# Kernel tuning notes

Hardware: AMD Instinct MI355X
Metric: run time of the kernel (lower is better)

Reference implementation:

```python
import jax, jax.numpy as jnp
import numpy as np

B, D, F = 16384, 512, 28
GIN = D + D + F + 1  # 1053
EPS = 1e-5


def setup_inputs() -> dict:
    key = jax.random.key(0)
    ks = jax.random.split(key, 16)
    s = 0.02
    return {
        "team_embedding": jax.random.normal(ks[0], (B, D), jnp.float32),
        "opponent_embedding": jax.random.normal(ks[1], (B, D), jnp.float32),
        "game_features": jax.random.normal(ks[2], (B, F), jnp.float32),
        "won": jnp.round(jax.random.uniform(ks[3], (B, 1), jnp.float32)),
        # input_projection Linear(GIN -> D)
        "W_proj": jax.random.normal(ks[4], (D, GIN), jnp.float32) * s,
        "b_proj": jnp.zeros((D,), jnp.float32),
        # GRUCell params (PyTorch layout: [3D, *] with r,z,n blocks)
        "W_ih": jax.random.normal(ks[5], (3 * D, D), jnp.float32) * s,
        "b_ih": jnp.zeros((3 * D,), jnp.float32),
        "W_hh": jax.random.normal(ks[6], (3 * D, D), jnp.float32) * s,
        "b_hh": jnp.zeros((3 * D,), jnp.float32),
        # LayerNorm
        "gamma": jnp.ones((D,), jnp.float32),
        "beta": jnp.zeros((D,), jnp.float32),
        # game_importance MLP: D -> 128 -> 1
        "W_imp1": jax.random.normal(ks[7], (128, D), jnp.float32) * s,
        "b_imp1": jnp.zeros((128,), jnp.float32),
        "W_imp2": jax.random.normal(ks[8], (1, 128), jnp.float32) * s,
        "b_imp2": jnp.zeros((1,), jnp.float32),
    }


def reference(team_embedding, opponent_embedding, game_features, won,
              W_proj, b_proj, W_ih, b_ih, W_hh, b_hh,
              gamma, beta, W_imp1, b_imp1, W_imp2, b_imp2):
    # combined: [B, 2D+F+1]
    x = jnp.concatenate([team_embedding, opponent_embedding, game_features, won], axis=-1)
    # input_projection: Linear -> ReLU (Dropout is identity in eval)
    projected = jax.nn.relu(x @ W_proj.T + b_proj)  # [B, D]
    # game_importance: Linear -> ReLU -> Linear -> Sigmoid
    importance = jax.nn.sigmoid(jax.nn.relu(projected @ W_imp1.T + b_imp1) @ W_imp2.T + b_imp2)  # [B, 1]
    # GRUCell (PyTorch math)
    gi = projected @ W_ih.T + b_ih          # [B, 3D]
    gh = team_embedding @ W_hh.T + b_hh     # [B, 3D]
    i_r, i_z, i_n = jnp.split(gi, 3, axis=-1)
    h_r, h_z, h_n = jnp.split(gh, 3, axis=-1)
    r = jax.nn.sigmoid(i_r + h_r)
    z = jax.nn.sigmoid(i_z + h_z)
    n = jnp.tanh(i_n + r * h_n)
    new_embedding = (1.0 - z) * n + z * team_embedding
    # gated blend
    updated = team_embedding + importance * (new_embedding - team_embedding)
    # LayerNorm
    mu = jnp.mean(updated, axis=-1, keepdims=True)
    var = jnp.mean(jnp.square(updated - mu), axis=-1, keepdims=True)
    updated = gamma * (updated - mu) * jax.lax.rsqrt(var + EPS) + beta
    game_context = jax.lax.stop_gradient(projected)  # .detach().clone()
    return (updated, game_context)
```

## Files before the change

kernel.cpp:

```cpp
#include <hip/hip_runtime.h>
#include <hip/hip_bf16.h>


#define NB 16384
#define GINP 1088

typedef __bf16 bf16x8 __attribute__((ext_vector_type(8)));
typedef float f32x4 __attribute__((ext_vector_type(4)));
typedef unsigned short ushort8 __attribute__((ext_vector_type(8)));

__device__ __forceinline__ void gload_lds16(const void* g, void* l) {
  __builtin_amdgcn_global_load_lds(
      (const __attribute__((address_space(1))) void*)g,
      (__attribute__((address_space(3))) void*)l, 16, 0, 0);
}
__device__ __forceinline__ float sigmoidf_(float x) { return 1.0f / (1.0f + expf(-x)); }
__device__ __forceinline__ float bf2f(unsigned short u) {
  unsigned int x = ((unsigned int)u) << 16;
  float f; __builtin_memcpy(&f, &x, 4); return f;
}

__global__ __launch_bounds__(256) void prep_x2(
    const float* __restrict__ team, const float* __restrict__ opp,
    const float* __restrict__ gf, const float* __restrict__ won,
    __hip_bfloat16* __restrict__ X) {
  long idx = (long)blockIdx.x * 256 + threadIdx.x;
  if (idx >= (long)NB * 136) return;
  const int r = (int)(idx / 136);
  const int c8 = (int)(idx % 136) * 8;
  float v[8];
  if (c8 < 512) {
    float4 a = *(const float4*)&team[(size_t)r * 512 + c8];
    float4 b = *(const float4*)&team[(size_t)r * 512 + c8 + 4];
    v[0]=a.x; v[1]=a.y; v[2]=a.z; v[3]=a.w; v[4]=b.x; v[5]=b.y; v[6]=b.z; v[7]=b.w;
  } else if (c8 < 1024) {
    float4 a = *(const float4*)&opp[(size_t)r * 512 + (c8 - 512)];
    float4 b = *(const float4*)&opp[(size_t)r * 512 + (c8 - 512) + 4];
    v[0]=a.x; v[1]=a.y; v[2]=a.z; v[3]=a.w; v[4]=b.x; v[5]=b.y; v[6]=b.z; v[7]=b.w;
  } else if (c8 < 1048) {
    const int g0 = c8 - 1024;
#pragma unroll
    for (int e = 0; e < 8; ++e) v[e] = gf[(size_t)r * 28 + g0 + e];
  } else if (c8 == 1048) {
    v[0] = gf[(size_t)r * 28 + 24]; v[1] = gf[(size_t)r * 28 + 25];
    v[2] = gf[(size_t)r * 28 + 26]; v[3] = gf[(size_t)r * 28 + 27];
    v[4] = won[r]; v[5] = 0.f; v[6] = 0.f; v[7] = 0.f;
  } else {
#pragma unroll
    for (int e = 0; e < 8; ++e) v[e] = 0.f;
  }
  __hip_bfloat16 h[8];
#pragma unroll
  for (int e = 0; e < 8; ++e) h[e] = __float2bfloat16(v[e]);
  *(uint4*)&X[(size_t)r * GINP + c8] = *(const uint4*)h;
}

__global__ __launch_bounds__(256) void prep_w2(
    const float* __restrict__ Wproj, const float* __restrict__ Wih,
    const float* __restrict__ Whh, const float* __restrict__ Wimp1,
    const float* __restrict__ bih, const float* __restrict__ bhh,
    __hip_bfloat16* __restrict__ Wpb, __hip_bfloat16* __restrict__ Wrz,
    __hip_bfloat16* __restrict__ Wn, __hip_bfloat16* __restrict__ Wimp1b,
    float* __restrict__ bcat) {
  long idx = (long)blockIdx.x * 256 + threadIdx.x;
  if (idx < 512L * 1088) {
    int r = (int)(idx / 1088), c = (int)(idx % 1088);
    Wpb[idx] = __float2bfloat16(c < 1053 ? Wproj[(size_t)r * 1053 + c] : 0.f);
    return;
  }
  idx -= 512L * 1088;
  if (idx < 1024L * 1024) {
    int q = (int)(idx >> 10), c = (int)(idx & 1023);
    float v = (c < 512) ? Wih[(size_t)q * 512 + c] : Whh[(size_t)q * 512 + (c - 512)];
    Wrz[idx] = __float2bfloat16(v);
    return;
  }
  idx -= 1024L * 1024;
  if (idx < 1024L * 512) {
    int q = (int)(idx / 512), c = (int)(idx % 512);
    float v = (q < 512) ? Wih[(size_t)(1024 + q) * 512 + c]
                        : Whh[(size_t)(1024 + q - 512) * 512 + c];
    Wn[idx] = __float2bfloat16(v);
    return;
  }
  idx -= 1024L * 512;
  if (idx < 128L * 512) { Wimp1b[idx] = __float2bfloat16(Wimp1[idx]); return; }
  idx -= 128L * 512;
  if (idx < 2048) {
    int j = (int)idx;
    float v;
    if (j < 1024) v = bih[j] + bhh[j];
    else if (j < 1536) v = bih[j];
    else v = bhh[j - 512];
    bcat[j] = v;
  }
}

template <int MODE>
__global__ __launch_bounds__(512, 1) void gemm_dp(
    const __hip_bfloat16* __restrict__ A0, int lda0,
    const __hip_bfloat16* __restrict__ A1, int lda1,
    const __hip_bfloat16* __restrict__ W0, const __hip_bfloat16* __restrict__ W1,
    const float* __restrict__ bias,
    float* __restrict__ Cf, __hip_bfloat16* __restrict__ Cb,
    int tilesN, int NT0) {
  __shared__ __align__(16) unsigned short ldsA[3 * 256 * 64];
  __shared__ __align__(16) unsigned short ldsB[3 * 128 * 64];

  const int tid = threadIdx.x;
  const int wid = tid >> 6, lane = tid & 63;
  const int wr = wid >> 1, wc = wid & 1;
  const int fl = lane & 15, kh = lane >> 4;

  int bid = blockIdx.x;
  {
    const int cpx = gridDim.x >> 3;
    bid = (bid & 7) * cpx + (bid >> 3);
  }
  const int tm = bid / tilesN, tn = bid % tilesN;
  const int m0 = tm * 256;

  const __hip_bfloat16* Wp;
  int ldw, NT;
  if (MODE == 0) {
    Wp = W0 + (size_t)tn * 128 * GINP; ldw = GINP; NT = NT0;
  } else {
    if (tn < 8) { Wp = W0 + (size_t)tn * 128 * 1024; ldw = 1024; NT = 16; }
    else        { Wp = W1 + (size_t)(tn - 8) * 128 * 512; ldw = 512; NT = 8; }
  }
  const float* bp = bias + tn * 128;

  const int prow_b = tid >> 3;
  const int gp = tid & 7;

  auto stageAB = [&](int s, int buf) {
    const int kW = s * 64;
    const __hip_bfloat16* Ap; int lda; int kA;
    if (MODE == 0) { Ap = A0; lda = lda0; kA = s * 64; }
    else if (tn < 8) {
      if (s < 8) { Ap = A0; lda = lda0; kA = s * 64; }
      else       { Ap = A1; lda = lda1; kA = (s - 8) * 64; }
    } else if (tn < 12) { Ap = A0; lda = lda0; kA = s * 64; }
    else                { Ap = A1; lda = lda1; kA = s * 64; }
    unsigned short* la = &ldsA[buf * (256 * 64)];
    unsigned short* lb = &ldsB[buf * (128 * 64)];
#pragma unroll
    for (int i = 0; i < 4; ++i) {
      const int prow = i * 64 + prow_b;
      const int gl = gp ^ (prow & 7);
      gload_lds16(Ap + (size_t)(m0 + prow) * lda + kA + gl * 8,
                  la + i * 4096 + wid * 512);
    }
#pragma unroll
    for (int i = 0; i < 2; ++i) {
      const int prow = i * 64 + prow_b;
      const int gl = gp ^ (prow & 7);
      gload_lds16(Wp + (size_t)prow * ldw + kW + gl * 8,
                  lb + i * 4096 + wid * 512);
    }
  };

  f32x4 acc[4][4];
#pragma unroll
  for (int m = 0; m < 4; ++m)
#pragma unroll
    for (int n = 0; n < 4; ++n) acc[m][n] = (f32x4){0.f, 0.f, 0.f, 0.f};

  stageAB(0, 0);
  stageAB(1, 1);

  for (int t = 0; t < NT; ++t) {
    const int cur = t % 3;
    if (t + 1 < NT) {
      asm volatile("s_waitcnt vmcnt(6)" ::: "memory");
    } else {
      asm volatile("s_waitcnt vmcnt(0)" ::: "memory");
    }
    __builtin_amdgcn_s_barrier();
    if (t + 2 < NT) stageAB(t + 2, (t + 2) % 3);

    const unsigned short* At = &ldsA[cur * (256 * 64)];
    const unsigned short* Bt = &ldsB[cur * (128 * 64)];
    bf16x8 af[2][4], bfr[2][4];
#pragma unroll
    for (int kk = 0; kk < 2; ++kk) {
#pragma unroll
      for (int m = 0; m < 4; ++m) {
        const int r = wr * 64 + m * 16 + fl;
        const int g = (kk * 4 + kh) ^ (r & 7);
        af[kk][m] = *(const bf16x8*)&At[r * 64 + g * 8];
      }
#pragma unroll
      for (int n = 0; n < 4; ++n) {
        const int r = wc * 64 + n * 16 + fl;
        const int g = (kk * 4 + kh) ^ (r & 7);
        bfr[kk][n] = *(const bf16x8*)&Bt[r * 64 + g * 8];
      }
    }
    __builtin_amdgcn_s_setprio(1);
#pragma unroll
    for (int kk = 0; kk < 2; ++kk)
#pragma unroll
      for (int m = 0; m < 4; ++m)
#pragma unroll
        for (int n = 0; n < 4; ++n)
          acc[m][n] = __builtin_amdgcn_mfma_f32_16x16x32_bf16(af[kk][m], bfr[kk][n], acc[m][n], 0, 0, 0);
    __builtin_amdgcn_s_setprio(0);
  }

#pragma unroll
  for (int m = 0; m < 4; ++m)
#pragma unroll
    for (int n = 0; n < 4; ++n)
#pragma unroll
      for (int j = 0; j < 4; ++j) {
        const int lrow = wr * 64 + m * 16 + kh * 4 + j;
        const int lcol = wc * 64 + n * 16 + fl;
        const size_t grow = (size_t)(m0 + lrow);
        float v = acc[m][n][j] + bp[lcol];
        if (MODE == 0) {
          v = fmaxf(v, 0.f);
          Cf[grow * 512 + tn * 128 + lcol] = v;
          Cb[grow * 512 + tn * 128 + lcol] = __float2bfloat16(v);
        } else {
          Cb[grow * 2048 + tn * 128 + lcol] = __float2bfloat16(v);
        }
      }
}

__global__ __launch_bounds__(256, 2) void gemm_imp(
    const __hip_bfloat16* __restrict__ A, const __hip_bfloat16* __restrict__ W,
    const float* __restrict__ bias, float* __restrict__ Cf) {
  __shared__ __align__(16) unsigned short ldsA[128 * 64];
  __shared__ __align__(16) unsigned short ldsB[128 * 64];
  const int tid = threadIdx.x;
  const int w = tid >> 6, lane = tid & 63;
  const int wr = w >> 1, wc = w & 1;
  const int fl = lane & 15, kh = lane >> 4;
  const int srow = lane >> 3, scol = (lane & 7) * 8;
  const int m0 = blockIdx.x * 128;

  f32x4 acc[4][4];
#pragma unroll
  for (int m = 0; m < 4; ++m)
#pragma unroll
    for (int n = 0; n < 4; ++n) acc[m][n] = (f32x4){0.f, 0.f, 0.f, 0.f};

  for (int kt = 0; kt < 8; ++kt) {
    const int k0 = kt * 64;
#pragma unroll
    for (int c = 0; c < 4; ++c) {
      const int rgrp = c * 4 + w;
      const int row = rgrp * 8 + srow;
      gload_lds16(A + (size_t)(m0 + row) * 512 + k0 + scol, (char*)ldsA + rgrp * 1024);
      gload_lds16(W + (size_t)row * 512 + k0 + scol, (char*)ldsB + rgrp * 1024);
    }
    __syncthreads();
#pragma unroll
    for (int kk = 0; kk < 2; ++kk) {
      bf16x8 af[4], bfr[4];
#pragma unroll
      for (int m = 0; m < 4; ++m)
        af[m] = *(const bf16x8*)&ldsA[(wr * 64 + m * 16 + fl) * 64 + kk * 32 + kh * 8];
#pragma unroll
      for (int n = 0; n < 4; ++n)
        bfr[n] = *(const bf16x8*)&ldsB[(wc * 64 + n * 16 + fl) * 64 + kk * 32 + kh * 8];
#pragma unroll
      for (int m = 0; m < 4; ++m)
#pragma unroll
        for (int n = 0; n < 4; ++n)
          acc[m][n] = __builtin_amdgcn_mfma_f32_16x16x32_bf16(af[m], bfr[n], acc[m][n], 0, 0, 0);
    }
    __syncthreads();
  }
#pragma unroll
  for (int m = 0; m < 4; ++m)
#pragma unroll
    for (int n = 0; n < 4; ++n)
#pragma unroll
      for (int j = 0; j < 4; ++j) {
        const int lrow = wr * 64 + m * 16 + kh * 4 + j;
        const int lcol = wc * 64 + n * 16 + fl;
        if (lcol < 128)
          Cf[(size_t)(m0 + lrow) * 128 + lcol] = fmaxf(acc[m][n][j] + bias[lcol], 0.f);
      }
}

__global__ __launch_bounds__(256) void imp_k(const float* __restrict__ h1,
                                             const float* __restrict__ w2,
                                             const float* __restrict__ b2,
                                             float* __restrict__ imp) {
  const int row = blockIdx.x * 4 + (threadIdx.x >> 6);
  const int lane = threadIdx.x & 63;
  float p = h1[(size_t)row * 128 + lane] * w2[lane] +
            h1[(size_t)row * 128 + 64 + lane] * w2[64 + lane];
#pragma unroll
  for (int off = 32; off; off >>= 1) p += __shfl_down(p, off);
  if (lane == 0) imp[row] = sigmoidf_(p + b2[0]);
}

__global__ __launch_bounds__(256) void fuse_final2(
    const float* __restrict__ team, const __hip_bfloat16* __restrict__ gg,
    const float* __restrict__ imp, const float* __restrict__ gamma,
    const float* __restrict__ beta, float* __restrict__ out) {
  const int row = blockIdx.x * 4 + (threadIdx.x >> 6);
  const int lane = threadIdx.x & 63;
  const size_t gb = (size_t)row * 2048 + lane * 8;
  ushort8 sr = *(const ushort8*)&gg[gb];
  ushort8 szv = *(const ushort8*)&gg[gb + 512];
  ushort8 inn = *(const ushort8*)&gg[gb + 1024];
  ushort8 hnn = *(const ushort8*)&gg[gb + 1536];
  float4 t0 = *(const float4*)&team[(size_t)row * 512 + lane * 8];
  float4 t1 = *(const float4*)&team[(size_t)row * 512 + lane * 8 + 4];
  const float im = imp[row];
  float tv[8] = {t0.x, t0.y, t0.z, t0.w, t1.x, t1.y, t1.z, t1.w};
  float u[8];
  float s = 0.f, ss = 0.f;
#pragma unroll
  for (int e = 0; e < 8; ++e) {
    const float rg = sigmoidf_(bf2f(sr[e]));
    const float zg = sigmoidf_(bf2f(szv[e]));
    const float ng = tanhf(bf2f(inn[e]) + rg * bf2f(hnn[e]));
    const float ne = (1.f - zg) * ng + zg * tv[e];
    const float uu = tv[e] + im * (ne - tv[e]);
    u[e] = uu; s += uu; ss += uu * uu;
  }
#pragma unroll
  for (int off = 32; off; off >>= 1) {
    s += __shfl_down(s, off);
    ss += __shfl_down(ss, off);
  }
  s = __shfl(s, 0); ss = __shfl(ss, 0);
  const float mu = s * (1.f / 512.f);
  const float inv = rsqrtf(ss * (1.f / 512.f) - mu * mu + 1e-5f);
  float4 g0 = *(const float4*)&gamma[lane * 8], g1 = *(const float4*)&gamma[lane * 8 + 4];
  float4 b0 = *(const float4*)&beta[lane * 8], b1 = *(const float4*)&beta[lane * 8 + 4];
  float gv[8] = {g0.x, g0.y, g0.z, g0.w, g1.x, g1.y, g1.z, g1.w};
  float bv[8] = {b0.x, b0.y, b0.z, b0.w, b1.x, b1.y, b1.z, b1.w};
  float4 o0, o1;
  o0.x = gv[0] * (u[0] - mu) * inv + bv[0];
  o0.y = gv[1] * (u[1] - mu) * inv + bv[1];
  o0.z = gv[2] * (u[2] - mu) * inv + bv[2];
  o0.w = gv[3] * (u[3] - mu) * inv + bv[3];
  o1.x = gv[4] * (u[4] - mu) * inv + bv[4];
  o1.y = gv[5] * (u[5] - mu) * inv + bv[5];
  o1.z = gv[6] * (u[6] - mu) * inv + bv[6];
  o1.w = gv[7] * (u[7] - mu) * inv + bv[7];
  *(float4*)&out[(size_t)row * 512 + lane * 8] = o0;
  *(float4*)&out[(size_t)row * 512 + lane * 8 + 4] = o1;
}

extern "C" void kernel_launch(void* const* d_in, const int* in_sizes, int n_in,
                              void* d_out, int out_size, void* d_ws, size_t ws_size,
                              hipStream_t stream) {
  const float* team   = (const float*)d_in[0];
  const float* opp    = (const float*)d_in[1];
  const float* gf     = (const float*)d_in[2];
  const float* won    = (const float*)d_in[3];
  const float* W_proj = (const float*)d_in[4];
  const float* b_proj = (const float*)d_in[5];
  const float* W_ih   = (const float*)d_in[6];
  const float* b_ih   = (const float*)d_in[7];
  const float* W_hh   = (const float*)d_in[8];
  const float* b_hh   = (const float*)d_in[9];
  const float* gamma  = (const float*)d_in[10];
  const float* beta   = (const float*)d_in[11];
  const float* W_imp1 = (const float*)d_in[12];
  const float* b_imp1 = (const float*)d_in[13];
  const float* W_imp2 = (const float*)d_in[14];
  const float* b_imp2 = (const float*)d_in[15];

  char* ws = (char*)d_ws;
  size_t o = 0;
  __hip_bfloat16* Xbf    = (__hip_bfloat16*)(ws + o); o += (size_t)NB * GINP * 2;
  __hip_bfloat16* Wpb    = (__hip_bfloat16*)(ws + o); o += (size_t)512 * GINP * 2;
  __hip_bfloat16* Wrz    = (__hip_bfloat16*)(ws + o); o += (size_t)1024 * 1024 * 2;
  __hip_bfloat16* Wn     = (__hip_bfloat16*)(ws + o); o += (size_t)1024 * 512 * 2;
  __hip_bfloat16* Wimp1b = (__hip_bfloat16*)(ws + o); o += (size_t)128 * 512 * 2;
  float*          bcat   = (float*)(ws + o);          o += (size_t)2048 * 4;
  __hip_bfloat16* Pbf    = (__hip_bfloat16*)(ws + o); o += (size_t)NB * 512 * 2;
  float*          h1     = (float*)(ws + o);          o += (size_t)NB * 128 * 4;
  float*          imp    = (float*)(ws + o);          o += (size_t)NB * 4;
  __hip_bfloat16* gg     = (__hip_bfloat16*)(ws + o); o += (size_t)NB * 2048 * 2;

  float* out_updated = (float*)d_out;
  float* out_ctx     = (float*)d_out + (size_t)NB * 512;

  prep_x2<<<(NB * 136 + 255) / 256, 256, 0, stream>>>(team, opp, gf, won, Xbf);
  {
    const long total = 512L * 1088 + 1024L * 1024 + 1024L * 512 + 128L * 512 + 2048;
    prep_w2<<<(int)((total + 255) / 256), 256, 0, stream>>>(
        W_proj, W_ih, W_hh, W_imp1, b_ih, b_hh, Wpb, Wrz, Wn, Wimp1b, bcat);
  }
  gemm_dp<0><<<256, 512, 0, stream>>>(Xbf, GINP, nullptr, 0, Wpb, nullptr, b_proj,
                                      out_ctx, Pbf, 4, 17);
  gemm_imp<<<NB / 128, 256, 0, stream>>>(Pbf, Wimp1b, b_imp1, h1);
  imp_k<<<NB / 4, 256, 0, stream>>>(h1, W_imp2, b_imp2, imp);
  gemm_dp<2><<<1024, 512, 0, stream>>>(Pbf, 512, Xbf, GINP, Wrz, Wn, bcat,
                                       nullptr, gg, 16, 0);
  fuse_final2<<<NB / 4, 256, 0, stream>>>(team, gg, imp, gamma, beta, out_updated);
}
```

Before: 177.0 us.

## Enlarge GEMM tiles to 256x256 with 8-phase interleaved load/MFMA schedule

Both GEMM launches now use 256x256 output tiles instead of 256x128, with 8 waves in a 2x4 layout and 128 accumulator floats per thread. The main loop is double-buffered and split into four sub-phases, each interleaving LDS fragment reads, partial global-to-LDS staging of the next tiles, and a quarter of the MFMAs, with barriers between phases. The aim is more data reuse per LDS byte and better overlap of memory traffic with matrix math. In exchange it raises register pressure and halves the grid: 128 blocks for the projection GEMM, which may underfill the CUs, and 512 for the gate GEMM.

Result: slower. 195.2 us (+10.3%).

```diff
diff --git a/kernel.cpp b/kernel.cpp
--- a/kernel.cpp
+++ b/kernel.cpp
@@ -97,133 +97,171 @@
 }
 
 template <int MODE>
-__global__ __launch_bounds__(512, 1) void gemm_dp(
+__global__ __launch_bounds__(512, 1) void gemm_8p(
     const __hip_bfloat16* __restrict__ A0, int lda0,
     const __hip_bfloat16* __restrict__ A1, int lda1,
     const __hip_bfloat16* __restrict__ W0, const __hip_bfloat16* __restrict__ W1,
     const float* __restrict__ bias,
     float* __restrict__ Cf, __hip_bfloat16* __restrict__ Cb,
-    int tilesN, int NT0) {
-  __shared__ __align__(16) unsigned short ldsA[3 * 256 * 64];
-  __shared__ __align__(16) unsigned short ldsB[3 * 128 * 64];
+    int tilesN, int NTP) {
+  __shared__ __align__(16) unsigned short ldsA[2 * 256 * 64];
+  __shared__ __align__(16) unsigned short ldsB[2 * 256 * 64];
 
   const int tid = threadIdx.x;
   const int wid = tid >> 6, lane = tid & 63;
-  const int wr = wid >> 1, wc = wid & 1;
+  const int wr = wid >> 2, wc = wid & 3;
   const int fl = lane & 15, kh = lane >> 4;
+  const int gp = lane & 7, rsub = lane >> 3;
 
   int bid = blockIdx.x;
-  {
-    const int cpx = gridDim.x >> 3;
-    bid = (bid & 7) * cpx + (bid >> 3);
-  }
+  { const int cpx = gridDim.x >> 3; bid = (bid & 7) * cpx + (bid >> 3); }
   const int tm = bid / tilesN, tn = bid % tilesN;
   const int m0 = tm * 256;
 
-  const __hip_bfloat16* Wp;
-  int ldw, NT;
-  if (MODE == 0) {
-    Wp = W0 + (size_t)tn * 128 * GINP; ldw = GINP; NT = NT0;
-  } else {
-    if (tn < 8) { Wp = W0 + (size_t)tn * 128 * 1024; ldw = 1024; NT = 16; }
-    else        { Wp = W1 + (size_t)(tn - 8) * 128 * 512; ldw = 512; NT = 8; }
-  }
-  const float* bp = bias + tn * 128;
-
-  const int prow_b = tid >> 3;
-  const int gp = tid & 7;
-
-  auto stageAB = [&](int s, int buf) {
-    const int kW = s * 64;
-    const __hip_bfloat16* Ap; int lda; int kA;
-    if (MODE == 0) { Ap = A0; lda = lda0; kA = s * 64; }
-    else if (tn < 8) {
-      if (s < 8) { Ap = A0; lda = lda0; kA = s * 64; }
-      else       { Ap = A1; lda = lda1; kA = (s - 8) * 64; }
-    } else if (tn < 12) { Ap = A0; lda = lda0; kA = s * 64; }
-    else                { Ap = A1; lda = lda1; kA = s * 64; }
-    unsigned short* la = &ldsA[buf * (256 * 64)];
-    unsigned short* lb = &ldsB[buf * (128 * 64)];
-#pragma unroll
-    for (int i = 0; i < 4; ++i) {
-      const int prow = i * 64 + prow_b;
-      const int gl = gp ^ (prow & 7);
-      gload_lds16(Ap + (size_t)(m0 + prow) * lda + kA + gl * 8,
-                  la + i * 4096 + wid * 512);
-    }
-#pragma unroll
-    for (int i = 0; i < 2; ++i) {
-      const int prow = i * 64 + prow_b;
-      const int gl = gp ^ (prow & 7);
-      gload_lds16(Wp + (size_t)prow * ldw + kW + gl * 8,
-                  lb + i * 4096 + wid * 512);
+  const __hip_bfloat16* Wp; int ldw, NT;
+  if (MODE == 0) { Wp = W0 + (size_t)tn * 256 * GINP; ldw = GINP; NT = NTP; }
+  else {
+    if (tn < 4)      { Wp = W0 + (size_t)tn * 256 * 1024; ldw = 1024; NT = 16; }
+    else if (tn < 6) { Wp = W1 + (size_t)(tn - 4) * 256 * 512; ldw = 512; NT = 8; }
+    else             { Wp = W1 + (size_t)(512 + (tn - 6) * 256) * 512; ldw = 512; NT = 8; }
+  }
+  const float* bp = bias + tn * 256;
+
+  auto stageA = [&](int s, int half) {
+    const __hip_bfloat16* Ap; int lda; int k0;
+    if (MODE == 0) { Ap = A0; lda = lda0; k0 = s * 64; }
+    else if (tn < 4) {
+      if (s < 8) { Ap = A0; lda = lda0; k0 = s * 64; }
+      else       { Ap = A1; lda = lda1; k0 = (s - 8) * 64; }
+    } else if (tn < 6) { Ap = A0; lda = lda0; k0 = s * 64; }
+    else               { Ap = A1; lda = lda1; k0 = s * 64; }
+    unsigned short* base = &ldsA[(s & 1) * 16384];
+#pragma unroll
+    for (int c = 0; c < 2; ++c) {
+      const int r0 = half * 128 + c * 64;
+      const int row = r0 + wid * 8 + rsub;
+      const int gl = gp ^ (row & 7);
+      gload_lds16(Ap + (size_t)(m0 + row) * lda + k0 + gl * 8,
+                  base + (size_t)(r0 + wid * 8) * 64);
     }
   };
-
-  f32x4 acc[4][4];
-#pragma unroll
-  for (int m = 0; m < 4; ++m)
+  auto stageB = [&](int s, int half) {
+    const int kW = s * 64;
+    unsigned short* base = &ldsB[(s & 1) * 16384];
+#pragma unroll
+    for (int c = 0; c < 2; ++c) {
+      const int r0 = half * 128 + c * 64;
+      const int row = r0 + wid * 8 + rsub;
+      const int gl = gp ^ (row & 7);
+      gload_lds16(Wp + (size_t)row * ldw + kW + gl * 8,
+                  base + (size_t)(r0 + wid * 8) * 64);
+    }
+  };
+  auto readA = [&](const unsigned short* At, int m, int kk) -> bf16x8 {
+    const int row = wr * 128 + m * 16 + fl;
+    const int G = kk * 4 + kh;
+    return *(const bf16x8*)&At[row * 64 + ((G ^ (row & 7)) * 8)];
+  };
+  auto readB = [&](const unsigned short* Bt, int n, int kk) -> bf16x8 {
+    const int row = wc * 64 + n * 16 + fl;
+    const int G = kk * 4 + kh;
+    return *(const bf16x8*)&Bt[row * 64 + ((G ^ (row & 7)) * 8)];
+  };
+
+  f32x4 acc[8][4];
+#pragma unroll
+  for (int m = 0; m < 8; ++m)
 #pragma unroll
     for (int n = 0; n < 4; ++n) acc[m][n] = (f32x4){0.f, 0.f, 0.f, 0.f};
 
-  stageAB(0, 0);
-  stageAB(1, 1);
-
-  for (int t = 0; t < NT; ++t) {
-    const int cur = t % 3;
-    if (t + 1 < NT) {
-      asm volatile("s_waitcnt vmcnt(6)" ::: "memory");
-    } else {
-      asm volatile("s_waitcnt vmcnt(0)" ::: "memory");
-    }
-    __builtin_amdgcn_s_barrier();
-    if (t + 2 < NT) stageAB(t + 2, (t + 2) % 3);
-
-    const unsigned short* At = &ldsA[cur * (256 * 64)];
-    const unsigned short* Bt = &ldsB[cur * (128 * 64)];
-    bf16x8 af[2][4], bfr[2][4];
-#pragma unroll
-    for (int kk = 0; kk < 2; ++kk) {
-#pragma unroll
-      for (int m = 0; m < 4; ++m) {
-        const int r = wr * 64 + m * 16 + fl;
-        const int g = (kk * 4 + kh) ^ (r & 7);
-        af[kk][m] = *(const bf16x8*)&At[r * 64 + g * 8];
-      }
-#pragma unroll
-      for (int n = 0; n < 4; ++n) {
-        const int r = wc * 64 + n * 16 + fl;
-        const int g = (kk * 4 + kh) ^ (r & 7);
-        bfr[kk][n] = *(const bf16x8*)&Bt[r * 64 + g * 8];
-      }
-    }
+  stageA(0, 0); stageA(0, 1); stageB(0, 0); stageB(0, 1);
+  stageA(1, 0); stageA(1, 1);
+  asm volatile("s_waitcnt vmcnt(4)" ::: "memory");
+  __builtin_amdgcn_s_barrier();
+
+  for (int T = 0; T < NT; ++T) {
+    const unsigned short* At = &ldsA[(T & 1) * 16384];
+    const unsigned short* Bt = &ldsB[(T & 1) * 16384];
+    bf16x8 fa0[4][2], fa1[4][2], fb0[2][2], fb1[2][2];
+
+#pragma unroll
+    for (int m = 0; m < 4; ++m) { fa0[m][0] = readA(At, m, 0); fa0[m][1] = readA(At, m, 1); }
+#pragma unroll
+    for (int n = 0; n < 2; ++n) { fb0[n][0] = readB(Bt, n, 0); fb0[n][1] = readB(Bt, n, 1); }
+    if (T + 1 < NT) { stageB(T + 1, 0); stageB(T + 1, 1); }
+    __builtin_amdgcn_s_barrier();
     __builtin_amdgcn_s_setprio(1);
 #pragma unroll
     for (int kk = 0; kk < 2; ++kk)
 #pragma unroll
       for (int m = 0; m < 4; ++m)
 #pragma unroll
-        for (int n = 0; n < 4; ++n)
-          acc[m][n] = __builtin_amdgcn_mfma_f32_16x16x32_bf16(af[kk][m], bfr[kk][n], acc[m][n], 0, 0, 0);
+        for (int n = 0; n < 2; ++n)
+          acc[m][n] = __builtin_amdgcn_mfma_f32_16x16x32_bf16(fa0[m][kk], fb0[n][kk], acc[m][n], 0, 0, 0);
     __builtin_amdgcn_s_setprio(0);
-  }
-
-#pragma unroll
-  for (int m = 0; m < 4; ++m)
+    __builtin_amdgcn_s_barrier();
+
+#pragma unroll
+    for (int m = 0; m < 4; ++m) { fa1[m][0] = readA(At, m + 4, 0); fa1[m][1] = readA(At, m + 4, 1); }
+    __builtin_amdgcn_s_barrier();
+    __builtin_amdgcn_s_setprio(1);
+#pragma unroll
+    for (int kk = 0; kk < 2; ++kk)
+#pragma unroll
+      for (int m = 0; m < 4; ++m)
+#pragma unroll
+        for (int n = 0; n < 2; ++n)
+          acc[m + 4][n] = __builtin_amdgcn_mfma_f32_16x16x32_bf16(fa1[m][kk], fb0[n][kk], acc[m + 4][n], 0, 0, 0);
+    __builtin_amdgcn_s_setprio(0);
+    __builtin_amdgcn_s_barrier();
+
+#pragma unroll
+    for (int n = 0; n < 2; ++n) { fb1[n][0] = readB(Bt, n + 2, 0); fb1[n][1] = readB(Bt, n + 2, 1); }
+    if (T + 2 < NT) stageA(T + 2, 0);
+    __builtin_amdgcn_s_barrier();
+    __builtin_amdgcn_s_setprio(1);
+#pragma unroll
+    for (int kk = 0; kk < 2; ++kk)
+#pragma unroll
+      for (int m = 0; m < 4; ++m)
+#pragma unroll
+        for (int n = 0; n < 2; ++n)
+          acc[m + 4][n + 2] = __builtin_amdgcn_mfma_f32_16x16x32_bf16(fa1[m][kk], fb1[n][kk], acc[m + 4][n + 2], 0, 0, 0);
+    __builtin_amdgcn_s_setprio(0);
+    __builtin_amdgcn_s_barrier();
+
+    if (T + 2 < NT) stageA(T + 2, 1);
+    __builtin_amdgcn_s_barrier();
+    __builtin_amdgcn_s_setprio(1);
+#pragma unroll
+    for (int kk = 0; kk < 2; ++kk)
+#pragma unroll
+      for (int m = 0; m < 4; ++m)
+#pragma unroll
+        for (int n = 0; n < 2; ++n)
+          acc[m][n + 2] = __builtin_amdgcn_mfma_f32_16x16x32_bf16(fa0[m][kk], fb1[n][kk], acc[m][n + 2], 0, 0, 0);
+    __builtin_amdgcn_s_setprio(0);
+    if (T + 2 < NT) { asm volatile("s_waitcnt vmcnt(4)" ::: "memory"); }
+    else            { asm volatile("s_waitcnt vmcnt(0)" ::: "memory"); }
+    __builtin_amdgcn_s_barrier();
+  }
+
+#pragma unroll
+  for (int m = 0; m < 8; ++m)
 #pragma unroll
     for (int n = 0; n < 4; ++n)
 #pragma unroll
       for (int j = 0; j < 4; ++j) {
-        const int lrow = wr * 64 + m * 16 + kh * 4 + j;
+        const int lrow = wr * 128 + m * 16 + kh * 4 + j;
         const int lcol = wc * 64 + n * 16 + fl;
         const size_t grow = (size_t)(m0 + lrow);
         float v = acc[m][n][j] + bp[lcol];
         if (MODE == 0) {
           v = fmaxf(v, 0.f);
-          Cf[grow * 512 + tn * 128 + lcol] = v;
-          Cb[grow * 512 + tn * 128 + lcol] = __float2bfloat16(v);
+          Cf[grow * 512 + tn * 256 + lcol] = v;
+          Cb[grow * 512 + tn * 256 + lcol] = __float2bfloat16(v);
         } else {
-          Cb[grow * 2048 + tn * 128 + lcol] = __float2bfloat16(v);
+          Cb[grow * 2048 + tn * 256 + lcol] = __float2bfloat16(v);
         }
       }
 }
@@ -392,11 +430,11 @@
     prep_w2<<<(int)((total + 255) / 256), 256, 0, stream>>>(
         W_proj, W_ih, W_hh, W_imp1, b_ih, b_hh, Wpb, Wrz, Wn, Wimp1b, bcat);
   }
-  gemm_dp<0><<<256, 512, 0, stream>>>(Xbf, GINP, nullptr, 0, Wpb, nullptr, b_proj,
-                                      out_ctx, Pbf, 4, 17);
+  gemm_8p<0><<<128, 512, 0, stream>>>(Xbf, GINP, nullptr, 0, Wpb, nullptr, b_proj,
+                                      out_ctx, Pbf, 2, 17);
   gemm_imp<<<NB / 128, 256, 0, stream>>>(Pbf, Wimp1b, b_imp1, h1);
   imp_k<<<NB / 4, 256, 0, stream>>>(h1, W_imp2, b_imp2, imp);
-  gemm_dp<2><<<1024, 512, 0, stream>>>(Pbf, 512, Xbf, GINP, Wrz, Wn, bcat,
-                                       nullptr, gg, 16, 0);
+  gemm_8p<2><<<512, 512, 0, stream>>>(Pbf, 512, Xbf, GINP, Wrz, Wn, bcat,
+                                      nullptr, gg, 8, 0);
   fuse_final2<<<NB / 4, 256, 0, stream>>>(team, gg, imp, gamma, beta, out_updated);
 }
```
